# Performance work log

Measured on AMD Instinct MI355X. Metric: run time of the kernel, lower is better.

The kernel has to match this reference:

```python
import jax, jax.numpy as jnp
import numpy as np

NUM_HEADS = 4
NUM_POINTS = 8


def deform_attn_3d(q, value, ref, Hf, Wf, Wv, bv, Wo, bo, Wa, ba):
    # q: (BS,N,C)  value: (BS,Hf*Wf,C)  ref: (BS,N,D,2) normalized (x,y) in [0,1]
    BS, N, C = q.shape
    H, P = NUM_HEADS, NUM_POINTS
    D = ref.shape[2]
    c = C // H
    # value projection, split heads: (BS,H,M,c)
    v = (value @ Wv + bv).reshape(BS, Hf * Wf, H, c).transpose(0, 2, 1, 3)
    # sampling offsets and attention weights from the query
    off = (q @ Wo + bo).reshape(BS, N, H, P, 2)
    attn = jax.nn.softmax((q @ Wa + ba).reshape(BS, N, H, P), axis=-1)
    # normalize offsets by (W,H); distribute P points over D z-anchors (P//D per anchor)
    norm = jnp.array([Wf, Hf], dtype=q.dtype)
    off = off.reshape(BS, N, H, P // D, D, 2) / norm
    loc = (ref[:, :, None, None, :, :] + off).reshape(BS, N, H, P, 2)
    # grid_sample(align_corners=False, padding=zeros): pixel = loc*size - 0.5
    x = loc[..., 0] * Wf - 0.5
    y = loc[..., 1] * Hf - 0.5
    x0f = jnp.floor(x)
    y0f = jnp.floor(y)
    lx = x - x0f
    ly = y - y0f
    x0 = x0f.astype(jnp.int32)
    y0 = y0f.astype(jnp.int32)

    def tohead(a):  # (BS,N,H,P) -> (BS,H,N*P)
        return a.transpose(0, 2, 1, 3).reshape(BS, H, N * P)

    def gather(yy, xx):
        valid = ((xx >= 0) & (xx < Wf) & (yy >= 0) & (yy < Hf)).astype(q.dtype)
        idx = jnp.clip(yy, 0, Hf - 1) * Wf + jnp.clip(xx, 0, Wf - 1)
        g = jnp.take_along_axis(v, tohead(idx)[..., None], axis=2)  # (BS,H,N*P,c)
        return g * tohead(valid)[..., None]

    out = (gather(y0, x0) * tohead((1 - lx) * (1 - ly))[..., None]
           + gather(y0, x0 + 1) * tohead(lx * (1 - ly))[..., None]
           + gather(y0 + 1, x0) * tohead((1 - lx) * ly)[..., None]
           + gather(y0 + 1, x0 + 1) * tohead(lx * ly)[..., None])
    out = (out * tohead(attn)[..., None]).reshape(BS, H, N, P, c).sum(3)  # (BS,H,N,c)
    return out.transpose(0, 2, 1, 3).reshape(BS, N, C)


def spatial_cross_attention(query, query_pos, value, reference_points_cam, bev_mask,
                            Hf, Wf, Wv, bv, Wo, bo, Wa, ba, Wout, bout):
    # query/query_pos: (B,N,C); value: (S,M,B,C); ref: (S,B,N,D,2); bev_mask: (S,B,N,D)
    B, N, C = query.shape
    S, M = value.shape[0], value.shape[1]
    D = reference_points_cam.shape[3]
    q = query + query_pos
    # broadcast queries over cameras (mask-equivalent of the torch rebatch/compaction):
    # deformable attention is per-query independent, so computing all queries per cam
    # and masking invalid ones is the same math as rebatch+scatter.
    q_all = jnp.broadcast_to(q[:, None], (B, S, N, C)).reshape(B * S, N, C)
    v_all = value.transpose(2, 0, 1, 3).reshape(B * S, M, C)
    ref = reference_points_cam.transpose(1, 0, 2, 3, 4).reshape(B * S, N, D, 2)
    out = deform_attn_3d(q_all, v_all, ref, Hf, Wf, Wv, bv, Wo, bo, Wa, ba)
    out = out.reshape(B, S, N, C)
    mask_q = (bev_mask.sum(-1) > 0).astype(query.dtype)  # (S,B,N): query hits this cam
    slots = (out * mask_q.transpose(1, 0, 2)[..., None]).sum(1)  # (B,N,C)
    count = jnp.maximum(mask_q.sum(0), 1.0)  # (B,N) clamp(min=1)
    slots = slots / count[..., None]
    # output_proj, dropout (eval -> identity), residual with original query
    return slots @ Wout + bout + query


def setup_inputs() -> dict:
    B, S, N, Z, C = 1, 6, 16384, 8, 128
    Hf, Wf = 28, 50
    H, P = NUM_HEADS, NUM_POINTS
    rng = jax.random.key(0)
    ks = jax.random.split(rng, 12)
    return {
        "query": jax.random.normal(ks[0], (B, N, C), jnp.float32),
        "query_pos": 0.1 * jax.random.normal(ks[1], (B, N, C), jnp.float32),
        "value": jax.random.normal(ks[2], (S, Hf * Wf, B, C), jnp.float32),
        "reference_points_cam": jax.random.uniform(ks[3], (S, B, N, Z, 2), jnp.float32),
        "bev_mask": jax.random.randint(ks[4], (S, B, N, Z), 0, 2).astype(bool),
        "Wv": 0.02 * jax.random.normal(ks[5], (C, C), jnp.float32),
        "bv": jnp.zeros((C,), jnp.float32),
        "Wo": 0.02 * jax.random.normal(ks[6], (C, H * P * 2), jnp.float32),
        "bo": 0.5 * jax.random.normal(ks[7], (H * P * 2,), jnp.float32),
        "Wa": 0.02 * jax.random.normal(ks[8], (C, H * P), jnp.float32),
        "ba": jnp.zeros((H * P,), jnp.float32),
        "Wout": 0.02 * jax.random.normal(ks[9], (C, C), jnp.float32),
        "bout": jnp.zeros((C,), jnp.float32),
        "Hf": Hf,
        "Wf": Wf,
    }


def reference(query, query_pos, value, reference_points_cam, bev_mask,
              Wv, bv, Wo, bo, Wa, ba, Wout, bout, Hf, Wf):
    return spatial_cross_attention(query, query_pos, value, reference_points_cam, bev_mask,
                                   Hf, Wf, Wv, bv, Wo, bo, Wa, ba, Wout, bout)
```

## Files before the change

### kernel.cpp

```cpp
#include <hip/hip_runtime.h>
#include <hip/hip_fp16.h>

#define N_Q   16384
#define C_DIM 128
#define S_CAM 6
#define M_VAL 1400
#define D_Z   8
#define HF    28
#define WF    50
#define QPB   16

__device__ __forceinline__ bool mask_any(const unsigned char* __restrict__ mask,
                                         int mflag, size_t mbase){
  if(mflag==0){
    int any=0;
    #pragma unroll
    for(int d=0;d<D_Z;d++) any |= mask[mbase+d];
    return any!=0;
  } else if(mflag==1){
    const int* mp = (const int*)mask;  int any=0;
    #pragma unroll
    for(int d=0;d<D_Z;d++) any |= mp[mbase+d];
    return any!=0;
  } else {
    const long long* mp = (const long long*)mask;  long long any=0;
    #pragma unroll
    for(int d=0;d<D_Z;d++) any |= mp[mbase+d];
    return any!=0;
  }
}

__global__ __launch_bounds__(256)
void value_proj_kernel(const float* __restrict__ value,
                       const float* __restrict__ Wv,
                       const float* __restrict__ bv,
                       unsigned short* __restrict__ vh16,
                       const unsigned char* __restrict__ mask,
                       int* __restrict__ flag){
  __shared__ float tile[8][C_DIM];
  __shared__ int s_cntA, s_cntB;
  const int tid = threadIdx.x;
  const int col = tid & 127;
  const int rh  = tid >> 7;
  const int r0  = blockIdx.x * 8;
  if(blockIdx.x==0 && tid==0){ s_cntA=0; s_cntB=0; }
  {
    const float4* src = (const float4*)(value + (size_t)r0*C_DIM);
    ((float4*)&tile[0][0])[tid] = src[tid];
  }
  __syncthreads();
  float acc[4];
  const float bias = bv[col];
  #pragma unroll
  for(int r=0;r<4;r++) acc[r]=bias;
  for(int k=0;k<C_DIM;k+=4){
    const float w0 = Wv[(k+0)*C_DIM + col];
    const float w1 = Wv[(k+1)*C_DIM + col];
    const float w2 = Wv[(k+2)*C_DIM + col];
    const float w3 = Wv[(k+3)*C_DIM + col];
    #pragma unroll
    for(int r=0;r<4;r++){
      const float4 t = *(const float4*)&tile[rh*4+r][k];
      acc[r] += t.x*w0 + t.y*w1 + t.z*w2 + t.w*w3;
    }
  }
  #pragma unroll
  for(int r=0;r<4;r++)
    vh16[(size_t)(r0+rh*4+r)*C_DIM + col] =
        __half_as_ushort(__float2half_rn(acc[r]));
  if(blockIdx.x==0){
    int a=0, b=0;
    for(int i=tid;i<1024;i+=256){
      const unsigned char v = mask[i];
      if(((i&3)!=0) && v) a=1;
      if(((i&7)==4) && v) b=1;
    }
    if(a) atomicOr(&s_cntA,1);
    if(b) atomicOr(&s_cntB,1);
    __syncthreads();
    if(tid==0) flag[0] = s_cntA ? 0 : (s_cntB ? 1 : 2);
  }
}

__global__ __launch_bounds__(256)
void fused_deform_kernel(const unsigned short* __restrict__ vh16,
                         const float* __restrict__ query,
                         const float* __restrict__ query_pos,
                         const float* __restrict__ Wo, const float* __restrict__ bo,
                         const float* __restrict__ Wa, const float* __restrict__ ba,
                         const float* __restrict__ ref,
                         const unsigned char* __restrict__ mask,
                         const int* __restrict__ flag,
                         const float* __restrict__ Wout,
                         const float* __restrict__ bout,
                         float* __restrict__ out){
  __shared__ float  qs[QPB][C_DIM+4];
  __shared__ float  offs[QPB][68];
  __shared__ float  attns[QPB][36];
  __shared__ float  logits[QPB][36];
  __shared__ float2 refs[QPB][S_CAM*D_Z+1];
  __shared__ int    activ[QPB][S_CAM];
  __shared__ float  cinv[QPB];

  const int tid = threadIdx.x;
  const int n0  = blockIdx.x * QPB;
  const int mflag = flag[0];
  const int qi = tid >> 4;
  const int l  = tid & 15;

  float2 rpre[3];
  #pragma unroll
  for(int j=0;j<3;j++){
    const int e = tid + 256*j;
    const int q = e/48, r = e%48;
    rpre[j] = ((const float2*)ref)[((size_t)(r>>3)*N_Q + (n0+q))*D_Z + (r&7)];
  }

  {
    const float4* qa = (const float4*)(query     + (size_t)n0*C_DIM);
    const float4* qb = (const float4*)(query_pos + (size_t)n0*C_DIM);
    #pragma unroll
    for(int j=0;j<2;j++){
      const int idx = tid + 256*j;
      const int r = idx >> 5, c4 = idx & 31;
      float4 A = qa[idx], B = qb[idx];
      *(float4*)&qs[r][c4*4] = make_float4(A.x+B.x, A.y+B.y, A.z+B.z, A.w+B.w);
    }
  }
  __syncthreads();

  {
    float ao0 = bo[l*4+0], ao1 = bo[l*4+1], ao2 = bo[l*4+2], ao3 = bo[l*4+3];
    float aa0 = ba[l*2+0], aa1 = ba[l*2+1];
    for(int k=0;k<C_DIM;k++){
      const float qv = qs[qi][k];
      const float4 wo = *(const float4*)&Wo[k*64 + l*4];
      const float2 wa = *(const float2*)&Wa[k*32 + l*2];
      ao0 += qv*wo.x; ao1 += qv*wo.y; ao2 += qv*wo.z; ao3 += qv*wo.w;
      aa0 += qv*wa.x; aa1 += qv*wa.y;
    }
    offs[qi][l*4+0] = ao0;  offs[qi][l*4+1] = ao1;
    offs[qi][l*4+2] = ao2;  offs[qi][l*4+3] = ao3;
    logits[qi][l*2+0] = aa0;  logits[qi][l*2+1] = aa1;
  }
  #pragma unroll
  for(int j=0;j<3;j++){
    const int e = tid + 256*j;
    refs[e/48][e%48] = rpre[j];
  }
  if(tid < QPB*S_CAM){
    const int q2 = tid / S_CAM, s = tid % S_CAM;
    activ[q2][s] = mask_any(mask, mflag, ((size_t)s*N_Q + (n0+q2))*D_Z) ? 1 : 0;
  }
  __syncthreads();
  if(tid < 64){
    const int q2 = tid >> 2, h = tid & 3;
    const float* L = &logits[q2][h*8];
    float mx = L[0];
    #pragma unroll
    for(int p=1;p<8;p++) mx = fmaxf(mx, L[p]);
    float e[8], ssum = 0.f;
    #pragma unroll
    for(int p=0;p<8;p++){ e[p] = __expf(L[p]-mx); ssum += e[p]; }
    const float inv = 1.f/ssum;
    #pragma unroll
    for(int p=0;p<8;p++) attns[q2][h*8+p] = e[p]*inv;
  } else if(tid >= 256-QPB){
    const int q2 = tid - (256-QPB);
    int c = 0;
    #pragma unroll
    for(int s=0;s<S_CAM;s++) c += activ[q2][s];
    cinv[q2] = 1.f / fmaxf((float)c, 1.f);
  }
  __syncthreads();

  const int gh  = l >> 2;
  const int gch = gh*32 + (l&3)*8;
  __half2 acc0 = __float2half2_rn(0.f);
  __half2 acc1 = acc0, acc2 = acc0, acc3 = acc0;

  for(int s=0;s<S_CAM;s++){
    if(!activ[qi][s]) continue;
    const unsigned short* vb = vh16 + (size_t)s*M_VAL*C_DIM + gch;
    #pragma unroll 2
    for(int p=0;p<8;p++){
      const float2 r2 = refs[qi][s*8+p];
      const float ox = offs[qi][gh*16+p*2+0];
      const float oy = offs[qi][gh*16+p*2+1];
      const float x = fmaf(r2.x, (float)WF, ox - 0.5f);
      const float y = fmaf(r2.y, (float)HF, oy - 0.5f);
      const float x0f = floorf(x), y0f = floorf(y);
      const float fx = x - x0f,    fy = y - y0f;
      const int x0 = (int)x0f, y0 = (int)y0f;
      const int x1 = x0+1,     y1 = y0+1;
      const float at = attns[qi][gh*8+p];
      const float wx0 = (x0>=0 && x0<WF) ? (1.f-fx) : 0.f;
      const float wx1 = (x1>=0 && x1<WF) ? fx       : 0.f;
      const float wy0 = ((y0>=0 && y0<HF) ? (1.f-fy) : 0.f) * at;
      const float wy1 = ((y1>=0 && y1<HF) ? fy       : 0.f) * at;
      const int x0c = min(max(x0,0), WF-1), x1c = min(max(x1,0), WF-1);
      const int y0c = min(max(y0,0), HF-1), y1c = min(max(y1,0), HF-1);
      const __half2 W00 = __float2half2_rn(wx0*wy0);
      const __half2 W01 = __float2half2_rn(wx1*wy0);
      const __half2 W10 = __float2half2_rn(wx0*wy1);
      const __half2 W11 = __float2half2_rn(wx1*wy1);
      const uint4 v00 = *(const uint4*)(vb + (y0c*WF+x0c)*C_DIM);
      const uint4 v01 = *(const uint4*)(vb + (y0c*WF+x1c)*C_DIM);
      const uint4 v10 = *(const uint4*)(vb + (y1c*WF+x0c)*C_DIM);
      const uint4 v11 = *(const uint4*)(vb + (y1c*WF+x1c)*C_DIM);
      #define H2(u) (*reinterpret_cast<const __half2*>(&(u)))
      acc0 = __hfma2(H2(v00.x), W00, acc0);  acc0 = __hfma2(H2(v01.x), W01, acc0);
      acc0 = __hfma2(H2(v10.x), W10, acc0);  acc0 = __hfma2(H2(v11.x), W11, acc0);
      acc1 = __hfma2(H2(v00.y), W00, acc1);  acc1 = __hfma2(H2(v01.y), W01, acc1);
      acc1 = __hfma2(H2(v10.y), W10, acc1);  acc1 = __hfma2(H2(v11.y), W11, acc1);
      acc2 = __hfma2(H2(v00.z), W00, acc2);  acc2 = __hfma2(H2(v01.z), W01, acc2);
      acc2 = __hfma2(H2(v10.z), W10, acc2);  acc2 = __hfma2(H2(v11.z), W11, acc2);
      acc3 = __hfma2(H2(v00.w), W00, acc3);  acc3 = __hfma2(H2(v01.w), W01, acc3);
      acc3 = __hfma2(H2(v10.w), W10, acc3);  acc3 = __hfma2(H2(v11.w), W11, acc3);
      #undef H2
    }
  }

  __syncthreads();
  {
    const float inv = cinv[qi];
    *(float4*)&qs[qi][gch]   = make_float4(__low2float(acc0)*inv, __high2float(acc0)*inv,
                                           __low2float(acc1)*inv, __high2float(acc1)*inv);
    *(float4*)&qs[qi][gch+4] = make_float4(__low2float(acc2)*inv, __high2float(acc2)*inv,
                                           __low2float(acc3)*inv, __high2float(acc3)*inv);
  }
  __syncthreads();
  {
    const int c0 = l*8;
    const int n  = n0 + qi;
    const float4 bA = *(const float4*)&bout[c0];
    const float4 bB = *(const float4*)&bout[c0+4];
    const float4 rA = *(const float4*)&query[(size_t)n*C_DIM + c0];
    const float4 rB = *(const float4*)&query[(size_t)n*C_DIM + c0 + 4];
    float o0=bA.x+rA.x, o1=bA.y+rA.y, o2=bA.z+rA.z, o3=bA.w+rA.w;
    float o4=bB.x+rB.x, o5=bB.y+rB.y, o6=bB.z+rB.z, o7=bB.w+rB.w;
    for(int k=0;k<C_DIM;k++){
      const float sv = qs[qi][k];
      const float4 wA = *(const float4*)&Wout[(size_t)k*C_DIM + c0];
      const float4 wB = *(const float4*)&Wout[(size_t)k*C_DIM + c0 + 4];
      o0 += sv*wA.x; o1 += sv*wA.y; o2 += sv*wA.z; o3 += sv*wA.w;
      o4 += sv*wB.x; o5 += sv*wB.y; o6 += sv*wB.z; o7 += sv*wB.w;
    }
    *(float4*)&out[(size_t)n*C_DIM + c0]     = make_float4(o0,o1,o2,o3);
    *(float4*)&out[(size_t)n*C_DIM + c0 + 4] = make_float4(o4,o5,o6,o7);
  }
}

extern "C" void kernel_launch(void* const* d_in, const int* in_sizes, int n_in,
                              void* d_out, int out_size, void* d_ws, size_t ws_size,
                              hipStream_t stream){
  const float* query     = (const float*)d_in[0];
  const float* query_pos = (const float*)d_in[1];
  const float* value     = (const float*)d_in[2];
  const float* ref       = (const float*)d_in[3];
  const unsigned char* mask = (const unsigned char*)d_in[4];
  const float* Wv   = (const float*)d_in[5];
  const float* bv   = (const float*)d_in[6];
  const float* Wo   = (const float*)d_in[7];
  const float* bo   = (const float*)d_in[8];
  const float* Wa   = (const float*)d_in[9];
  const float* ba   = (const float*)d_in[10];
  const float* Wout = (const float*)d_in[11];
  const float* bout = (const float*)d_in[12];
  float* out = (float*)d_out;

  int* flag = (int*)d_ws;
  unsigned short* vh16 = (unsigned short*)((char*)d_ws + 64);

  value_proj_kernel<<<(S_CAM*M_VAL)/8, 256, 0, stream>>>(value, Wv, bv, vh16, mask, flag);
  fused_deform_kernel<<<N_Q/QPB, 256, 0, stream>>>(vh16, query, query_pos,
                                                   Wo, bo, Wa, ba, ref, mask, flag,
                                                   Wout, bout, out);
}
```

Measured before the change: 193.5 us.

## Halve queries per block and split camera loop across two thread groups

Reduces queries per block from 16 to 8 and gives each query 32 threads instead of 16. The per-query sampling loop over six cameras is split so each 16-thread subgroup handles three cameras, and the two partial sums are combined through shared memory before the output projection. The goal is twice as many blocks and shorter per-thread serial gather chains, for better latency hiding and load balance. In exchange it adds an extra barrier and reduction step, and the weight matrices are reloaded across twice as many blocks.

Result: no change. 197.3 us (+2.0%).

```diff
diff --git a/kernel.cpp b/kernel.cpp
--- a/kernel.cpp
+++ b/kernel.cpp
@@ -8,7 +8,7 @@
 #define D_Z   8
 #define HF    28
 #define WF    50
-#define QPB   16
+#define QPB   8
 
 __device__ __forceinline__ bool mask_any(const unsigned char* __restrict__ mask,
                                          int mflag, size_t mbase){
@@ -105,55 +105,53 @@
   const int tid = threadIdx.x;
   const int n0  = blockIdx.x * QPB;
   const int mflag = flag[0];
-  const int qi = tid >> 4;
-  const int l  = tid & 15;
-
-  float2 rpre[3];
-  #pragma unroll
-  for(int j=0;j<3;j++){
-    const int e = tid + 256*j;
+  const int qi = tid >> 5;
+  const int l  = tid & 31;
+
+  float2 rpre0, rpre1;
+  {
+    const int e = tid;
     const int q = e/48, r = e%48;
-    rpre[j] = ((const float2*)ref)[((size_t)(r>>3)*N_Q + (n0+q))*D_Z + (r&7)];
+    rpre0 = ((const float2*)ref)[((size_t)(r>>3)*N_Q + (n0+q))*D_Z + (r&7)];
+  }
+  if(tid < 128){
+    const int e = tid + 256;
+    const int q = e/48, r = e%48;
+    rpre1 = ((const float2*)ref)[((size_t)(r>>3)*N_Q + (n0+q))*D_Z + (r&7)];
   }
 
   {
     const float4* qa = (const float4*)(query     + (size_t)n0*C_DIM);
     const float4* qb = (const float4*)(query_pos + (size_t)n0*C_DIM);
-    #pragma unroll
-    for(int j=0;j<2;j++){
-      const int idx = tid + 256*j;
-      const int r = idx >> 5, c4 = idx & 31;
-      float4 A = qa[idx], B = qb[idx];
-      *(float4*)&qs[r][c4*4] = make_float4(A.x+B.x, A.y+B.y, A.z+B.z, A.w+B.w);
-    }
-  }
-  __syncthreads();
-
-  {
-    float ao0 = bo[l*4+0], ao1 = bo[l*4+1], ao2 = bo[l*4+2], ao3 = bo[l*4+3];
-    float aa0 = ba[l*2+0], aa1 = ba[l*2+1];
+    const int r = tid >> 5, c4 = tid & 31;
+    float4 A = qa[tid], B = qb[tid];
+    *(float4*)&qs[r][c4*4] = make_float4(A.x+B.x, A.y+B.y, A.z+B.z, A.w+B.w);
+  }
+  __syncthreads();
+
+  {
+    float ao0 = bo[l*2+0], ao1 = bo[l*2+1];
+    float aa0 = ba[l];
     for(int k=0;k<C_DIM;k++){
       const float qv = qs[qi][k];
-      const float4 wo = *(const float4*)&Wo[k*64 + l*4];
-      const float2 wa = *(const float2*)&Wa[k*32 + l*2];
-      ao0 += qv*wo.x; ao1 += qv*wo.y; ao2 += qv*wo.z; ao3 += qv*wo.w;
-      aa0 += qv*wa.x; aa1 += qv*wa.y;
-    }
-    offs[qi][l*4+0] = ao0;  offs[qi][l*4+1] = ao1;
-    offs[qi][l*4+2] = ao2;  offs[qi][l*4+3] = ao3;
-    logits[qi][l*2+0] = aa0;  logits[qi][l*2+1] = aa1;
-  }
-  #pragma unroll
-  for(int j=0;j<3;j++){
-    const int e = tid + 256*j;
-    refs[e/48][e%48] = rpre[j];
+      const float2 wo = *(const float2*)&Wo[k*64 + l*2];
+      ao0 += qv*wo.x; ao1 += qv*wo.y;
+      aa0 += qv*Wa[k*32 + l];
+    }
+    offs[qi][l*2+0] = ao0;  offs[qi][l*2+1] = ao1;
+    logits[qi][l]   = aa0;
+  }
+  refs[tid/48][tid%48] = rpre0;
+  if(tid < 128){
+    const int e = tid + 256;
+    refs[e/48][e%48] = rpre1;
   }
   if(tid < QPB*S_CAM){
     const int q2 = tid / S_CAM, s = tid % S_CAM;
     activ[q2][s] = mask_any(mask, mflag, ((size_t)s*N_Q + (n0+q2))*D_Z) ? 1 : 0;
   }
   __syncthreads();
-  if(tid < 64){
+  if(tid < 32){
     const int q2 = tid >> 2, h = tid & 3;
     const float* L = &logits[q2][h*8];
     float mx = L[0];
@@ -174,12 +172,14 @@
   }
   __syncthreads();
 
-  const int gh  = l >> 2;
-  const int gch = gh*32 + (l&3)*8;
+  const int sg  = l >> 4;
+  const int ll  = l & 15;
+  const int gh  = ll >> 2;
+  const int gch = gh*32 + (ll&3)*8;
   __half2 acc0 = __float2half2_rn(0.f);
   __half2 acc1 = acc0, acc2 = acc0, acc3 = acc0;
 
-  for(int s=0;s<S_CAM;s++){
+  for(int s=sg*3; s<sg*3+3; s++){
     if(!activ[qi][s]) continue;
     const unsigned short* vb = vh16 + (size_t)s*M_VAL*C_DIM + gch;
     #pragma unroll 2
@@ -221,33 +221,38 @@
     }
   }
 
-  __syncthreads();
-  {
+  const float4 partA = make_float4(__low2float(acc0), __high2float(acc0),
+                                   __low2float(acc1), __high2float(acc1));
+  const float4 partB = make_float4(__low2float(acc2), __high2float(acc2),
+                                   __low2float(acc3), __high2float(acc3));
+  __syncthreads();
+  if(sg==0){
+    *(float4*)&qs[qi][gch]   = partA;
+    *(float4*)&qs[qi][gch+4] = partB;
+  }
+  __syncthreads();
+  if(sg==1){
     const float inv = cinv[qi];
-    *(float4*)&qs[qi][gch]   = make_float4(__low2float(acc0)*inv, __high2float(acc0)*inv,
-                                           __low2float(acc1)*inv, __high2float(acc1)*inv);
-    *(float4*)&qs[qi][gch+4] = make_float4(__low2float(acc2)*inv, __high2float(acc2)*inv,
-                                           __low2float(acc3)*inv, __high2float(acc3)*inv);
-  }
-  __syncthreads();
-  {
-    const int c0 = l*8;
+    float4 pA = *(const float4*)&qs[qi][gch];
+    float4 pB = *(const float4*)&qs[qi][gch+4];
+    *(float4*)&qs[qi][gch]   = make_float4((pA.x+partA.x)*inv, (pA.y+partA.y)*inv,
+                                           (pA.z+partA.z)*inv, (pA.w+partA.w)*inv);
+    *(float4*)&qs[qi][gch+4] = make_float4((pB.x+partB.x)*inv, (pB.y+partB.y)*inv,
+                                           (pB.z+partB.z)*inv, (pB.w+partB.w)*inv);
+  }
+  __syncthreads();
+  {
+    const int c0 = l*4;
     const int n  = n0 + qi;
-    const float4 bA = *(const float4*)&bout[c0];
-    const float4 bB = *(const float4*)&bout[c0+4];
-    const float4 rA = *(const float4*)&query[(size_t)n*C_DIM + c0];
-    const float4 rB = *(const float4*)&query[(size_t)n*C_DIM + c0 + 4];
-    float o0=bA.x+rA.x, o1=bA.y+rA.y, o2=bA.z+rA.z, o3=bA.w+rA.w;
-    float o4=bB.x+rB.x, o5=bB.y+rB.y, o6=bB.z+rB.z, o7=bB.w+rB.w;
+    const float4 b4 = *(const float4*)&bout[c0];
+    const float4 r4 = *(const float4*)&query[(size_t)n*C_DIM + c0];
+    float o0=b4.x+r4.x, o1=b4.y+r4.y, o2=b4.z+r4.z, o3=b4.w+r4.w;
     for(int k=0;k<C_DIM;k++){
       const float sv = qs[qi][k];
-      const float4 wA = *(const float4*)&Wout[(size_t)k*C_DIM + c0];
-      const float4 wB = *(const float4*)&Wout[(size_t)k*C_DIM + c0 + 4];
-      o0 += sv*wA.x; o1 += sv*wA.y; o2 += sv*wA.z; o3 += sv*wA.w;
-      o4 += sv*wB.x; o5 += sv*wB.y; o6 += sv*wB.z; o7 += sv*wB.w;
-    }
-    *(float4*)&out[(size_t)n*C_DIM + c0]     = make_float4(o0,o1,o2,o3);
-    *(float4*)&out[(size_t)n*C_DIM + c0 + 4] = make_float4(o4,o5,o6,o7);
+      const float4 w = *(const float4*)&Wout[(size_t)k*C_DIM + c0];
+      o0 += sv*w.x; o1 += sv*w.y; o2 += sv*w.z; o3 += sv*w.w;
+    }
+    *(float4*)&out[(size_t)n*C_DIM + c0] = make_float4(o0,o1,o2,o3);
   }
 }
 
```
